# Kernel optimization log

Hardware: AMD Instinct MI355X
Metric: run time of the kernel (lower is better)

Reference implementation:

```python
import jax, jax.numpy as jnp
import numpy as np
import math

N_HEADS = 16
ROPE_THETA = 10000.0
NEG_INF = -1e30


def setup_inputs() -> dict:
    key = jax.random.key(0)
    k1, k2, k3, k4 = jax.random.split(key, 4)
    B, S, D = 2, 2048, 2048
    x = jax.random.normal(k1, (B, S, D), dtype=jnp.float32)
    qkv = 0.01 * jax.random.normal(k2, (2 * D, D), dtype=jnp.float32)
    H = N_HEADS
    dh = D // H
    nope = dh // 2
    rope = dh // 2
    wk = 0.01 * jax.random.normal(k3, (H * nope + rope, D), dtype=jnp.float32)
    wo = 0.01 * jax.random.normal(k4, (D, D), dtype=jnp.float32)
    return {"x": x, "qkv": qkv, "wk": wk, "wo": wo}


def _rope_cos_sin(S, dh, rope_dim, dtype):
    # freqs over full dh as in the torch module, then sliced to rope_dim//2 and tiled x2
    freqs = 1.0 / (ROPE_THETA ** (jnp.arange(0, dh, 2).astype(jnp.float32) / dh))
    emb = jnp.arange(S, dtype=jnp.float32)[:, None] * freqs[None, :]  # [S, dh//2]
    cos = jnp.tile(jnp.cos(emb)[:, : rope_dim // 2], (1, 2))[None, None]  # [1,1,S,rope]
    sin = jnp.tile(jnp.sin(emb)[:, : rope_dim // 2], (1, 2))[None, None]
    return cos.astype(dtype), sin.astype(dtype)


def _apply_rope(xq, cos, sin):
    x1, x2 = jnp.split(xq, 2, axis=-1)
    return xq * cos + jnp.concatenate([-x2, x1], axis=-1) * sin


def reference(x, qkv, wk, wo):
    B, S, D = x.shape
    H = N_HEADS
    dh = D // H
    nope = dh // 2
    rope = dh // 2

    QV = x @ qkv.T                              # [B,S,2D]
    Q, V = jnp.split(QV, 2, axis=-1)
    Q = Q.reshape(B, S, H, dh).transpose(0, 2, 1, 3)        # [B,H,S,dh]
    v_heads = V.reshape(B, S, H, dh).transpose(0, 2, 1, 3)  # [B,H,S,dh]
    Qn, Qr = Q[..., :nope], Q[..., nope:]

    K = x @ wk.T                                # [B,S,H*nope+rope]
    Kn = K[..., : H * nope].reshape(B, S, H, nope).transpose(0, 2, 1, 3)  # [B,H,S,nope]
    Kr = K[..., H * nope :].reshape(B, S, 1, rope).transpose(0, 2, 1, 3)  # [B,1,S,rope]

    cos, sin = _rope_cos_sin(S, dh, rope, x.dtype)
    Qr = _apply_rope(Qr, cos, sin)
    Kr = _apply_rope(Kr, cos, sin)

    q_heads = jnp.concatenate([Qn, Qr], axis=-1)                               # [B,H,S,dh]
    k_heads = jnp.concatenate([Kn, jnp.broadcast_to(Kr, (B, H, S, rope))], -1)  # [B,H,S,dh]

    scale = 1.0 / math.sqrt(dh)
    scores = jnp.einsum('bhqd,bhkd->bhqk', q_heads, k_heads) * scale
    mask = jnp.tril(jnp.ones((S, S), dtype=bool))
    scores = jnp.where(mask[None, None], scores, NEG_INF)
    attn = jax.nn.softmax(scores, axis=-1)
    out = jnp.einsum('bhqk,bhkd->bhqd', attn, v_heads)
    out = out.transpose(0, 2, 1, 3).reshape(B, S, D) @ wo.T
    return (out, k_heads, v_heads)
```

## Files before the change

### kernel.cpp

```cpp
#include <hip/hip_runtime.h>
#include <hip/hip_bf16.h>


typedef unsigned short u16;
typedef unsigned int u32;
typedef __bf16 bf16x8 __attribute__((ext_vector_type(8)));
typedef float f32x4 __attribute__((ext_vector_type(4)));

__device__ __forceinline__ u16 f2bf(float x) {
  union { __hip_bfloat16 h; u16 u; } c;
  c.h = __float2bfloat16(x);
  return c.u;
}
__device__ __forceinline__ float bf2f(u16 u) {
  union { u32 u; float f; } c;
  c.u = ((u32)u) << 16;
  return c.f;
}
__device__ __forceinline__ u32 pack2(float a, float b) {
  return (u32)f2bf(a) | ((u32)f2bf(b) << 16);
}
__device__ __forceinline__ f32x4 mfma16(bf16x8 a, bf16x8 b, f32x4 c) {
  return __builtin_amdgcn_mfma_f32_16x16x32_bf16(a, b, c, 0, 0, 0);
}
__device__ __forceinline__ void gload_lds16(const void* g, void* l) {
  __builtin_amdgcn_global_load_lds((__attribute__((address_space(1))) void*)g,
                                   (__attribute__((address_space(3))) void*)l,
                                   16, 0, 0);
}

__global__ __launch_bounds__(256) void cast_all(const float4* __restrict__ x,
                                                const float4* __restrict__ qkv,
                                                const float* __restrict__ wk,
                                                const float4* __restrict__ wo,
                                                u16* __restrict__ x_bf,
                                                u16* __restrict__ wcomb,
                                                u16* __restrict__ wo_bf) {
  int i = blockIdx.x * blockDim.x + threadIdx.x;
  const float4* src;
  u16* dst;
  int j;
  if (i < 2097152) {
    src = x; dst = x_bf; j = i;
  } else if (i < 4194304) {
    src = qkv; dst = wcomb; j = i - 2097152;
  } else if (i < 4849664) {
    j = i - 4194304;
    int r = (j * 4) >> 11;
    u32 lo = 0, hi = 0;
    if (r < 1088) {
      float4 v = ((const float4*)wk)[j];
      lo = pack2(v.x, v.y);
      hi = pack2(v.z, v.w);
    }
    ((uint2*)(wcomb + 8388608))[j] = make_uint2(lo, hi);
    return;
  } else {
    src = wo; dst = wo_bf; j = i - 4849664;
  }
  float4 v = src[j];
  ((uint2*)dst)[j] = make_uint2(pack2(v.x, v.y), pack2(v.z, v.w));
}

__device__ __forceinline__ void cstore(u16* C, size_t i, float v) { C[i] = f2bf(v); }
__device__ __forceinline__ void cstore(float* C, size_t i, float v) { C[i] = v; }

template <typename CT, int BM, int BN>
__global__ __launch_bounds__(512, 2) void gemm256(const u16* __restrict__ A,
                                                  const u16* __restrict__ W,
                                                  CT* __restrict__ C,
                                                  int M, int N, int K) {
  constexpr int MI = BM / 64;
  constexpr int NI = BN / 128;
  constexpr int AH = BM * 64;
  constexpr int BH = BN * 64;
  constexpr int AL = BM / 128;
  constexpr int BL = BN / 128;
  constexpr int BOFF = 4 * AH;
  __shared__ char lds[BOFF + 4 * BH];
  const int tid = threadIdx.x;
  const int wid = tid >> 6, lane = tid & 63;
  const int lr = lane & 15, lg = lane >> 4;
  const int wr = wid >> 2, wc = wid & 3;
  const int xorv = (lr & 7) << 4;
  const int nwg = gridDim.x * gridDim.y;
  const int lin = blockIdx.y * gridDim.x + blockIdx.x;
  const int swz = (lin & 7) * (nwg >> 3) + (lin >> 3);
  const int m0 = (swz / gridDim.x) * BM;
  const int n0 = (swz % gridDim.x) * BN;
  const int nkt = K >> 6;

  f32x4 acc[2 * MI][2 * NI] = {};
  bf16x8 a[MI][2], b[2 * NI][2];

  const int o0 = tid * 16, o1 = 8192 + tid * 16;
  const int r0 = o0 >> 7, c0 = ((o0 & 127) ^ ((r0 & 7) << 4)) >> 1;
  const int r1 = o1 >> 7, c1 = ((o1 & 127) ^ ((r1 & 7) << 4)) >> 1;
  const u16* gA0[2] = {A + (size_t)(m0 + r0) * K + c0,
                       A + (size_t)(m0 + BM / 2 + r0) * K + c0};
  const u16* gA1[2] = {A + (size_t)(m0 + r1) * K + c1,
                       A + (size_t)(m0 + BM / 2 + r1) * K + c1};
  const u16* gB0[2] = {W + (size_t)(n0 + r0) * K + c0,
                       W + (size_t)(n0 + BN / 2 + r0) * K + c0};
  const u16* gB1[2] = {W + (size_t)(n0 + r1) * K + c1,
                       W + (size_t)(n0 + BN / 2 + r1) * K + c1};

  auto STAGEA = [&](int t, int h) {
    char* d_ = lds + (t & 1) * (2 * AH) + h * AH + wid * 1024;
    gload_lds16(gA0[h] + (size_t)t * 64, d_);
    if constexpr (AL == 2) gload_lds16(gA1[h] + (size_t)t * 64, d_ + 8192);
  };
  auto STAGEB = [&](int t, int h) {
    char* d_ = lds + BOFF + (t & 1) * (2 * BH) + h * BH + wid * 1024;
    gload_lds16(gB0[h] + (size_t)t * 64, d_);
    if constexpr (BL == 2) gload_lds16(gB1[h] + (size_t)t * 64, d_ + 8192);
  };
  auto WAITKEEP = [&]() {
    if constexpr (AL + BL == 4) asm volatile("s_waitcnt vmcnt(4)" ::: "memory");
    else asm volatile("s_waitcnt vmcnt(3)" ::: "memory");
  };

  STAGEA(0, 0); STAGEB(0, 0); STAGEA(0, 1); STAGEB(0, 1);
  if (nkt > 1) { STAGEA(1, 0); STAGEB(1, 0); }
  WAITKEEP();
  __builtin_amdgcn_s_barrier();

  for (int t = 0; t < nkt; ++t) {
    const char* Ab = lds + (t & 1) * (2 * AH);
    const char* Bb = lds + BOFF + (t & 1) * (2 * BH);
    const int arow = wr * (BM / 4), brow = wc * (BN / 8);
#pragma unroll
    for (int mi = 0; mi < MI; mi++)
#pragma unroll
      for (int ks = 0; ks < 2; ks++)
        a[mi][ks] = *(const bf16x8*)(Ab + (arow + mi * 16 + lr) * 128 + ((lg * 16 + ks * 64) ^ xorv));
#pragma unroll
    for (int ni = 0; ni < NI; ni++)
#pragma unroll
      for (int ks = 0; ks < 2; ks++)
        b[ni][ks] = *(const bf16x8*)(Bb + (brow + ni * 16 + lr) * 128 + ((lg * 16 + ks * 64) ^ xorv));
    if (t + 1 < nkt) STAGEA(t + 1, 1);
    __builtin_amdgcn_s_barrier();
    asm volatile("s_waitcnt lgkmcnt(0)" ::: "memory");
    __builtin_amdgcn_sched_barrier(0);
    __builtin_amdgcn_s_setprio(1);
#pragma unroll
    for (int mi = 0; mi < MI; mi++)
#pragma unroll
      for (int ni = 0; ni < NI; ni++)
#pragma unroll
        for (int ks = 0; ks < 2; ks++)
          acc[mi][ni] = mfma16(a[mi][ks], b[ni][ks], acc[mi][ni]);
    __builtin_amdgcn_s_setprio(0);
    __builtin_amdgcn_s_barrier();
#pragma unroll
    for (int ni = 0; ni < NI; ni++)
#pragma unroll
      for (int ks = 0; ks < 2; ks++)
        b[NI + ni][ks] = *(const bf16x8*)(Bb + BH + (brow + ni * 16 + lr) * 128 + ((lg * 16 + ks * 64) ^ xorv));
    if (t + 1 < nkt) STAGEB(t + 1, 1);
    __builtin_amdgcn_s_barrier();
    asm volatile("s_waitcnt lgkmcnt(0)" ::: "memory");
    __builtin_amdgcn_sched_barrier(0);
    __builtin_amdgcn_s_setprio(1);
#pragma unroll
    for (int mi = 0; mi < MI; mi++)
#pragma unroll
      for (int ni = 0; ni < NI; ni++)
#pragma unroll
        for (int ks = 0; ks < 2; ks++)
          acc[mi][NI + ni] = mfma16(a[mi][ks], b[NI + ni][ks], acc[mi][NI + ni]);
    __builtin_amdgcn_s_setprio(0);
    __builtin_amdgcn_s_barrier();
#pragma unroll
    for (int mi = 0; mi < MI; mi++)
#pragma unroll
      for (int ks = 0; ks < 2; ks++)
        a[mi][ks] = *(const bf16x8*)(Ab + AH + (arow + mi * 16 + lr) * 128 + ((lg * 16 + ks * 64) ^ xorv));
    if (t + 2 < nkt) STAGEA(t + 2, 0);
    __builtin_amdgcn_s_barrier();
    asm volatile("s_waitcnt lgkmcnt(0)" ::: "memory");
    __builtin_amdgcn_sched_barrier(0);
    __builtin_amdgcn_s_setprio(1);
#pragma unroll
    for (int mi = 0; mi < MI; mi++)
#pragma unroll
      for (int ni = 0; ni < NI; ni++)
#pragma unroll
        for (int ks = 0; ks < 2; ks++)
          acc[MI + mi][ni] = mfma16(a[mi][ks], b[ni][ks], acc[MI + mi][ni]);
    __builtin_amdgcn_s_setprio(0);
    __builtin_amdgcn_s_barrier();
    if (t + 2 < nkt) {
      STAGEB(t + 2, 0);
      WAITKEEP();
    } else if (t + 1 < nkt) {
      asm volatile("s_waitcnt vmcnt(0)" ::: "memory");
    }
    __builtin_amdgcn_s_barrier();
    asm volatile("s_waitcnt lgkmcnt(0)" ::: "memory");
    __builtin_amdgcn_sched_barrier(0);
    __builtin_amdgcn_s_setprio(1);
#pragma unroll
    for (int mi = 0; mi < MI; mi++)
#pragma unroll
      for (int ni = 0; ni < NI; ni++)
#pragma unroll
        for (int ks = 0; ks < 2; ks++)
          acc[MI + mi][NI + ni] = mfma16(a[mi][ks], b[NI + ni][ks], acc[MI + mi][NI + ni]);
    __builtin_amdgcn_s_setprio(0);
    __builtin_amdgcn_s_barrier();
  }

#pragma unroll
  for (int Mh = 0; Mh < 2; Mh++)
#pragma unroll
    for (int mi = 0; mi < MI; mi++) {
      int row = m0 + Mh * (BM / 2) + wr * (BM / 4) + mi * 16 + lg * 4;
#pragma unroll
      for (int Nh = 0; Nh < 2; Nh++)
#pragma unroll
        for (int ni = 0; ni < NI; ni++) {
          int col = n0 + Nh * (BN / 2) + wc * (BN / 8) + ni * 16 + lr;
#pragma unroll
          for (int r = 0; r < 4; r++)
            cstore(C, (size_t)(row + r) * N + col, acc[Mh * MI + mi][Nh * NI + ni][r]);
        }
    }
}

__global__ __launch_bounds__(256) void rope_scatter2(u16* __restrict__ QVK,
                                                     u16* __restrict__ kh,
                                                     float* __restrict__ k_out, int S) {
  const int row = blockIdx.x;
  const int b = row >> 11, s = row & 2047;
  const int tid = threadIdx.x;
  __shared__ float kr[64];
  const float LOG1E4_64 = 0.14391156511f;
  u16* qrow = QVK + (size_t)row * 5376;
  if (tid < 32) {
    float freq = __expf(-(float)tid * LOG1E4_64);
    float sn, c;
    __sincosf((float)s * freq, &sn, &c);
    float a = bf2f(qrow[5120 + tid]);
    float bb = bf2f(qrow[5152 + tid]);
    kr[tid] = a * c - bb * sn;
    kr[tid + 32] = bb * c + a * sn;
  }
  for (int idx = tid; idx < 512; idx += 256) {
    int h = idx >> 5, jj = idx & 31;
    float freq = __expf(-(float)jj * LOG1E4_64);
    float sn, c;
    __sincosf((float)s * freq, &sn, &c);
    u16* p1 = qrow + h * 128 + 64 + jj;
    u16* p2 = qrow + h * 128 + 96 + jj;
    float x1 = bf2f(*p1), x2 = bf2f(*p2);
    *p1 = f2bf(x1 * c - x2 * sn);
    *p2 = f2bf(x2 * c + x1 * sn);
  }
  __syncthreads();
  for (int idx = tid; idx < 2048; idx += 256) {
    int h = idx >> 7, d = idx & 127;
    float val = (d < 64) ? bf2f(qrow[4096 + h * 64 + d]) : kr[d - 64];
    size_t o = ((size_t)(b * 16 + h) * S + s) * 128 + d;
    kh[o] = f2bf(val);
    k_out[o] = val;
  }
}

__global__ __launch_bounds__(256) void v_scatter(const u16* __restrict__ QVK,
                                                 u16* __restrict__ vt,
                                                 float* __restrict__ v_out, int S) {
  const int blk = blockIdx.x;
  const int st = blk & 63;
  const int dt = (blk >> 6) & 3;
  const int bh = blk >> 8;
  const int b = bh >> 4, h = bh & 15;
  __shared__ u16 t[32][34];
  const int tx = threadIdx.x & 31, ty = threadIdx.x >> 5;
  const int s0 = st * 32, d0 = dt * 32;
#pragma unroll
  for (int i = 0; i < 4; i++) {
    int sl = ty + 8 * i;
    u16 u = QVK[(size_t)(b * S + s0 + sl) * 5376 + 2048 + h * 128 + d0 + tx];
    t[sl][tx] = u;
    v_out[((size_t)bh * S + s0 + sl) * 128 + d0 + tx] = bf2f(u);
  }
  __syncthreads();
#pragma unroll
  for (int i = 0; i < 4; i++) {
    int dl = ty + 8 * i;
    vt[((size_t)bh * 128 + d0 + dl) * S + s0 + tx] = t[tx][dl];
  }
}

__global__ __launch_bounds__(512) void flash_attn4(const u16* __restrict__ QVK,
                                                   const u16* __restrict__ Kh,
                                                   const u16* __restrict__ Vt,
                                                   u16* __restrict__ attn, int S) {
  __shared__ char lds[49152 + 8 * 2304];
  const int tid = threadIdx.x, wid = tid >> 6, lane = tid & 63;
  const int bh = blockIdx.x & 31;
  const int qb = 15 - (int)(blockIdx.x >> 5);
  const int q0 = qb * 128 + wid * 16;
  const int b = bh >> 4, h = bh & 15;
  const int q = lane & 15, g = lane >> 4;
  const u16* Qb = QVK + (size_t)b * S * 5376 + h * 128;
  const u16* Kb = Kh + (size_t)bh * S * 128;
  const u16* Vb = Vt + (size_t)bh * 128 * S;
  const int qg = q0 + q;
  const int xr = (q & 7) << 4;
  char* const Pw = lds + 49152 + wid * 2304 + q * 144;

  const u16* srcK[2];
  const u16* srcV[2];
#pragma unroll
  for (int i = 0; i < 2; i++) {
    int o = ((i * 8 + wid) << 10) | (lane << 4);
    int rK = o >> 8, cbK = (o & 255) ^ ((rK & 7) << 4);
    srcK[i] = Kb + rK * 128 + (cbK >> 1);
    int dV = o >> 7, kbV = (o & 127) ^ ((dV & 7) << 4);
    srcV[i] = Vb + (size_t)dV * S + (kbV >> 1);
  }

  bf16x8 qf[4];
#pragma unroll
  for (int f = 0; f < 4; f++)
    qf[f] = *(const bf16x8*)(Qb + (size_t)qg * 5376 + f * 32 + g * 8);

  f32x4 acc[8] = {};
  float m = -INFINITY, l = 0.f;
  const float sc = 0.08838834764831845f;
  const int ktiles = 2 * qb + 2;

#pragma unroll
  for (int i = 0; i < 2; i++) {
    char* ld = lds + ((i * 8 + wid) << 10);
    gload_lds16(srcK[i], ld);
    gload_lds16(srcV[i], ld + 32768);
  }
  asm volatile("s_waitcnt vmcnt(0)" ::: "memory");
  __builtin_amdgcn_s_barrier();

  for (int kt = 0; kt < ktiles; ++kt) {
    const char* Kt = lds + (kt & 1) * 16384;
    const char* Vl = lds + 32768;
    const bool more = (kt + 1 < ktiles);
    if (more) {
#pragma unroll
      for (int i = 0; i < 2; i++)
        gload_lds16(srcK[i] + (size_t)(kt + 1) * 8192,
                    lds + (((kt & 1) ^ 1) << 14) + ((i * 8 + wid) << 10));
      asm volatile("s_waitcnt vmcnt(4)" ::: "memory");
    } else {
      asm volatile("s_waitcnt vmcnt(2)" ::: "memory");
    }
    __builtin_amdgcn_s_barrier();

    f32x4 s[4] = {};
    const char* Kq = Kt + q * 256;
    __builtin_amdgcn_s_setprio(1);
#pragma unroll
    for (int f = 0; f < 4; f++) {
#pragma unroll
      for (int c = 0; c < 4; c++) {
        bf16x8 kf = *(const bf16x8*)(Kq + c * 4096 + ((f * 64 + g * 16) ^ xr));
        s[c] = mfma16(kf, qf[f], s[c]);
      }
    }
    __builtin_amdgcn_s_setprio(0);

    const int kbg = kt * 64;
    float v[16];
    const bool maskt = (kbg + 63 > q0);
#pragma unroll
    for (int c = 0; c < 4; c++)
#pragma unroll
      for (int r = 0; r < 4; r++) {
        float x = s[c][r];
        if (maskt && (kbg + c * 16 + g * 4 + r > qg)) x = -1e30f;
        v[c * 4 + r] = x;
      }
    float tm = v[0];
#pragma unroll
    for (int i = 1; i < 16; i++) tm = fmaxf(tm, v[i]);
    tm = fmaxf(tm, __shfl_xor(tm, 16));
    tm = fmaxf(tm, __shfl_xor(tm, 32));
    if (!__all(tm <= m + 64.0f)) {
      float mnew = fmaxf(m, tm);
      float corr = __expf((m - mnew) * sc);
      m = mnew;
      l *= corr;
      float corr_r[4];
#pragma unroll
      for (int r = 0; r < 4; r++)
        corr_r[r] = __shfl(corr, (lane & 48) | (g * 4 + r));
#pragma unroll
      for (int j = 0; j < 8; j++)
#pragma unroll
        for (int r = 0; r < 4; r++) acc[j][r] *= corr_r[r];
    }
    const float nms = -m * sc;
    float p[16], ts = 0.f;
#pragma unroll
    for (int i = 0; i < 16; i++) {
      p[i] = __expf(fmaf(v[i], sc, nms));
      ts += p[i];
    }
    ts += __shfl_xor(ts, 16);
    ts += __shfl_xor(ts, 32);
    l += ts;

#pragma unroll
    for (int c = 0; c < 4; c++) {
      int off = (c * 32 + g * 8) ^ xr;
      *(uint2*)(Pw + off) = make_uint2(pack2(p[c * 4], p[c * 4 + 1]),
                                       pack2(p[c * 4 + 2], p[c * 4 + 3]));
    }
    asm volatile("s_waitcnt lgkmcnt(0)" ::: "memory");
    __builtin_amdgcn_sched_barrier(0);
    bf16x8 pcA = *(const bf16x8*)(Pw + ((g * 16) ^ xr));
    bf16x8 pcB = *(const bf16x8*)(Pw + ((64 + g * 16) ^ xr));

    if (more) asm volatile("s_waitcnt vmcnt(2)" ::: "memory");
    else      asm volatile("s_waitcnt vmcnt(0)" ::: "memory");
    __builtin_amdgcn_s_barrier();

    const int vcolA = (g * 16) ^ xr;
    const int vcolB = (64 + g * 16) ^ xr;
    __builtin_amdgcn_s_setprio(1);
#pragma unroll
    for (int j = 0; j < 8; j++) {
      bf16x8 vfA = *(const bf16x8*)(Vl + (j * 16 + q) * 128 + vcolA);
      acc[j] = mfma16(pcA, vfA, acc[j]);
    }
#pragma unroll
    for (int j = 0; j < 8; j++) {
      bf16x8 vfB = *(const bf16x8*)(Vl + (j * 16 + q) * 128 + vcolB);
      acc[j] = mfma16(pcB, vfB, acc[j]);
    }
    __builtin_amdgcn_s_setprio(0);

    __builtin_amdgcn_s_barrier();
    if (more) {
#pragma unroll
      for (int i = 0; i < 2; i++)
        gload_lds16(srcV[i] + (size_t)(kt + 1) * 64,
                    lds + 32768 + ((i * 8 + wid) << 10));
    }
  }

  float linv = 1.0f / l;
  float linv_r[4];
#pragma unroll
  for (int r = 0; r < 4; r++)
    linv_r[r] = __shfl(linv, (lane & 48) | (g * 4 + r));
  u16* ab = attn + (size_t)(b * S + q0) * 2048 + h * 128;
#pragma unroll
  for (int j = 0; j < 8; j++)
#pragma unroll
    for (int r = 0; r < 4; r++)
      ab[(size_t)(g * 4 + r) * 2048 + j * 16 + q] = f2bf(acc[j][r] * linv_r[r]);
}

extern "C" void kernel_launch(void* const* d_in, const int* in_sizes, int n_in,
                              void* d_out, int out_size, void* d_ws, size_t ws_size,
                              hipStream_t stream) {
  (void)in_sizes; (void)n_in; (void)out_size; (void)ws_size;
  const int S = 2048;
  const float* x = (const float*)d_in[0];
  const float* qkv = (const float*)d_in[1];
  const float* wk = (const float*)d_in[2];
  const float* wo = (const float*)d_in[3];
  float* out = (float*)d_out;
  float* k_out = out + (size_t)8388608;
  float* v_out = out + (size_t)16777216;

  char* ws = (char*)d_ws;
  u16* x_bf  = (u16*)(ws + 0);
  u16* wcomb = (u16*)(ws + 16777216);
  u16* wo_bf = (u16*)(ws + 38797312);
  u16* qvk   = (u16*)(ws + 47185920);
  u16* vt_bf = (u16*)(ws + 91226112);
  u16* attn_bf = x_bf;
  u16* k_bf = wcomb;

  cast_all<<<23040, 256, 0, stream>>>((const float4*)x, (const float4*)qkv, wk,
                                      (const float4*)wo, x_bf, wcomb, wo_bf);

  gemm256<u16, 256, 256><<<dim3(16, 16), 512, 0, stream>>>(x_bf, wcomb, qvk,
                                                           4096, 5376, 2048);
  gemm256<u16, 256, 128><<<dim3(10, 16), 512, 0, stream>>>(
      x_bf, wcomb + (size_t)4096 * 2048, qvk + 4096, 4096, 5376, 2048);
  rope_scatter2<<<4096, 256, 0, stream>>>(qvk, k_bf, k_out, S);
  v_scatter<<<8192, 256, 0, stream>>>(qvk, vt_bf, v_out, S);
  flash_attn4<<<512, 512, 0, stream>>>(qvk, k_bf, vt_bf, attn_bf, S);
  gemm256<float, 128, 256><<<dim3(8, 32), 512, 0, stream>>>(attn_bf, wo_bf, out,
                                                            4096, 2048, 2048);
}
```

Baseline: 279.6 us.

## Rewrite flash attention with 32x32 MFMA tiles and 4 waves per block

The attention kernel moves from 16x16x32 to 32x32x16 bf16 MFMA. Each of 4 waves now handles 32 query rows instead of 8 waves handling 16 rows. P now stays in registers as the A operand rather than taking an LDS round trip, and waves skip fully masked causal tiles. The aim is fewer LDS reads per FLOP and less per-wave overhead. The cost is fewer waves per block, which may hurt latency hiding, and more register pressure from the larger accumulators.

Result: no change. 275.6 us (-1.4%).

```diff
diff --git a/kernel.cpp b/kernel.cpp
--- a/kernel.cpp
+++ b/kernel.cpp
@@ -6,6 +6,7 @@
 typedef unsigned int u32;
 typedef __bf16 bf16x8 __attribute__((ext_vector_type(8)));
 typedef float f32x4 __attribute__((ext_vector_type(4)));
+typedef float f32x16 __attribute__((ext_vector_type(16)));
 
 __device__ __forceinline__ u16 f2bf(float x) {
   union { __hip_bfloat16 h; u16 u; } c;
@@ -22,6 +23,9 @@
 }
 __device__ __forceinline__ f32x4 mfma16(bf16x8 a, bf16x8 b, f32x4 c) {
   return __builtin_amdgcn_mfma_f32_16x16x32_bf16(a, b, c, 0, 0, 0);
+}
+__device__ __forceinline__ f32x16 mfma32(bf16x8 a, bf16x8 b, f32x16 c) {
+  return __builtin_amdgcn_mfma_f32_32x32x16_bf16(a, b, c, 0, 0, 0);
 }
 __device__ __forceinline__ void gload_lds16(const void* g, void* l) {
   __builtin_amdgcn_global_load_lds((__attribute__((address_space(1))) void*)g,
@@ -294,48 +298,47 @@
   }
 }
 
-__global__ __launch_bounds__(512) void flash_attn4(const u16* __restrict__ QVK,
+__global__ __launch_bounds__(256) void flash_attn6(const u16* __restrict__ QVK,
                                                    const u16* __restrict__ Kh,
                                                    const u16* __restrict__ Vt,
                                                    u16* __restrict__ attn, int S) {
-  __shared__ char lds[49152 + 8 * 2304];
+  __shared__ char lds[49664];
   const int tid = threadIdx.x, wid = tid >> 6, lane = tid & 63;
   const int bh = blockIdx.x & 31;
   const int qb = 15 - (int)(blockIdx.x >> 5);
-  const int q0 = qb * 128 + wid * 16;
+  const int q0w = qb * 128 + wid * 32;
   const int b = bh >> 4, h = bh & 15;
-  const int q = lane & 15, g = lane >> 4;
+  const int r32 = lane & 31, hh = lane >> 5;
   const u16* Qb = QVK + (size_t)b * S * 5376 + h * 128;
   const u16* Kb = Kh + (size_t)bh * S * 128;
   const u16* Vb = Vt + (size_t)bh * 128 * S;
-  const int qg = q0 + q;
-  const int xr = (q & 7) << 4;
-  char* const Pw = lds + 49152 + wid * 2304 + q * 144;
-
-  const u16* srcK[2];
-  const u16* srcV[2];
-#pragma unroll
-  for (int i = 0; i < 2; i++) {
-    int o = ((i * 8 + wid) << 10) | (lane << 4);
+  const int qg = q0w + r32;
+  const int xr = (r32 & 7) << 4;
+  char* const Pc = lds + 49152 + wid * 128;
+
+  const u16 *srcK[4], *srcV[4];
+#pragma unroll
+  for (int i = 0; i < 4; i++) {
+    int o = i * 4096 + tid * 16;
     int rK = o >> 8, cbK = (o & 255) ^ ((rK & 7) << 4);
     srcK[i] = Kb + rK * 128 + (cbK >> 1);
     int dV = o >> 7, kbV = (o & 127) ^ ((dV & 7) << 4);
     srcV[i] = Vb + (size_t)dV * S + (kbV >> 1);
   }
 
-  bf16x8 qf[4];
-#pragma unroll
-  for (int f = 0; f < 4; f++)
-    qf[f] = *(const bf16x8*)(Qb + (size_t)qg * 5376 + f * 32 + g * 8);
-
-  f32x4 acc[8] = {};
+  bf16x8 qf[8];
+#pragma unroll
+  for (int f = 0; f < 8; f++)
+    qf[f] = *(const bf16x8*)(Qb + (size_t)qg * 5376 + f * 16 + hh * 8);
+
+  f32x16 acc[4] = {};
   float m = -INFINITY, l = 0.f;
   const float sc = 0.08838834764831845f;
   const int ktiles = 2 * qb + 2;
 
 #pragma unroll
-  for (int i = 0; i < 2; i++) {
-    char* ld = lds + ((i * 8 + wid) << 10);
+  for (int i = 0; i < 4; i++) {
+    char* ld = lds + i * 4096 + wid * 1024;
     gload_lds16(srcK[i], ld);
     gload_lds16(srcV[i], ld + 32768);
   }
@@ -348,119 +351,139 @@
     const bool more = (kt + 1 < ktiles);
     if (more) {
 #pragma unroll
-      for (int i = 0; i < 2; i++)
+      for (int i = 0; i < 4; i++)
         gload_lds16(srcK[i] + (size_t)(kt + 1) * 8192,
-                    lds + (((kt & 1) ^ 1) << 14) + ((i * 8 + wid) << 10));
+                    lds + (((kt & 1) ^ 1) << 14) + i * 4096 + wid * 1024);
+      asm volatile("s_waitcnt vmcnt(8)" ::: "memory");
+    } else {
       asm volatile("s_waitcnt vmcnt(4)" ::: "memory");
-    } else {
-      asm volatile("s_waitcnt vmcnt(2)" ::: "memory");
-    }
-    __builtin_amdgcn_s_barrier();
-
-    f32x4 s[4] = {};
-    const char* Kq = Kt + q * 256;
-    __builtin_amdgcn_s_setprio(1);
-#pragma unroll
-    for (int f = 0; f < 4; f++) {
-#pragma unroll
-      for (int c = 0; c < 4; c++) {
-        bf16x8 kf = *(const bf16x8*)(Kq + c * 4096 + ((f * 64 + g * 16) ^ xr));
-        s[c] = mfma16(kf, qf[f], s[c]);
+    }
+    __builtin_amdgcn_s_barrier();
+
+    const int kbg = kt * 64;
+    const bool active = (kbg <= q0w + 31);
+    u32 u[16];
+    if (active) {
+      f32x16 s[2] = {};
+      __builtin_amdgcn_s_setprio(1);
+#pragma unroll
+      for (int kg = 0; kg < 2; kg++) {
+        const char* Kq = Kt + (kg * 32 + r32) * 256;
+#pragma unroll
+        for (int f = 0; f < 8; f++) {
+          bf16x8 kf = *(const bf16x8*)(Kq + ((f * 32 + hh * 16) ^ xr));
+          s[kg] = mfma32(kf, qf[f], s[kg]);
+        }
       }
-    }
-    __builtin_amdgcn_s_setprio(0);
-
-    const int kbg = kt * 64;
-    float v[16];
-    const bool maskt = (kbg + 63 > q0);
-#pragma unroll
-    for (int c = 0; c < 4; c++)
-#pragma unroll
-      for (int r = 0; r < 4; r++) {
-        float x = s[c][r];
-        if (maskt && (kbg + c * 16 + g * 4 + r > qg)) x = -1e30f;
-        v[c * 4 + r] = x;
+      __builtin_amdgcn_s_setprio(0);
+      const bool maskt = (kbg + 63 > q0w);
+      if (maskt) {
+#pragma unroll
+        for (int kg = 0; kg < 2; kg++)
+#pragma unroll
+          for (int r = 0; r < 16; r++)
+            if (kbg + kg * 32 + (r & 3) + 8 * (r >> 2) + 4 * hh > qg)
+              s[kg][r] = -1e30f;
       }
-    float tm = v[0];
-#pragma unroll
-    for (int i = 1; i < 16; i++) tm = fmaxf(tm, v[i]);
-    tm = fmaxf(tm, __shfl_xor(tm, 16));
-    tm = fmaxf(tm, __shfl_xor(tm, 32));
-    if (!__all(tm <= m + 64.0f)) {
-      float mnew = fmaxf(m, tm);
-      float corr = __expf((m - mnew) * sc);
-      m = mnew;
-      l *= corr;
-      float corr_r[4];
-#pragma unroll
-      for (int r = 0; r < 4; r++)
-        corr_r[r] = __shfl(corr, (lane & 48) | (g * 4 + r));
-#pragma unroll
-      for (int j = 0; j < 8; j++)
-#pragma unroll
-        for (int r = 0; r < 4; r++) acc[j][r] *= corr_r[r];
-    }
-    const float nms = -m * sc;
-    float p[16], ts = 0.f;
-#pragma unroll
-    for (int i = 0; i < 16; i++) {
-      p[i] = __expf(fmaf(v[i], sc, nms));
-      ts += p[i];
-    }
-    ts += __shfl_xor(ts, 16);
-    ts += __shfl_xor(ts, 32);
-    l += ts;
-
-#pragma unroll
-    for (int c = 0; c < 4; c++) {
-      int off = (c * 32 + g * 8) ^ xr;
-      *(uint2*)(Pw + off) = make_uint2(pack2(p[c * 4], p[c * 4 + 1]),
-                                       pack2(p[c * 4 + 2], p[c * 4 + 3]));
-    }
-    asm volatile("s_waitcnt lgkmcnt(0)" ::: "memory");
-    __builtin_amdgcn_sched_barrier(0);
-    bf16x8 pcA = *(const bf16x8*)(Pw + ((g * 16) ^ xr));
-    bf16x8 pcB = *(const bf16x8*)(Pw + ((64 + g * 16) ^ xr));
-
-    if (more) asm volatile("s_waitcnt vmcnt(2)" ::: "memory");
+      float tm = s[0][0];
+#pragma unroll
+      for (int r = 1; r < 16; r++) tm = fmaxf(tm, s[0][r]);
+#pragma unroll
+      for (int r = 0; r < 16; r++) tm = fmaxf(tm, s[1][r]);
+      tm = fmaxf(tm, __shfl_xor(tm, 32));
+      if (!__all(tm <= m + 64.0f)) {
+        float mnew = fmaxf(m, tm);
+        float corr = __expf((m - mnew) * sc);
+        m = mnew;
+        l *= corr;
+        if (lane < 32) *(float*)(Pc + r32 * 4) = corr;
+        asm volatile("s_waitcnt lgkmcnt(0)" ::: "memory");
+        __builtin_amdgcn_sched_barrier(0);
+        f32x4 c0 = *(const f32x4*)(Pc + (4 * hh) * 4);
+        f32x4 c1 = *(const f32x4*)(Pc + (8 + 4 * hh) * 4);
+        f32x4 c2 = *(const f32x4*)(Pc + (16 + 4 * hh) * 4);
+        f32x4 c3 = *(const f32x4*)(Pc + (24 + 4 * hh) * 4);
+#pragma unroll
+        for (int dg = 0; dg < 4; dg++)
+#pragma unroll
+          for (int r = 0; r < 16; r++) {
+            float cr = (r >> 2) == 0 ? c0[r & 3]
+                     : (r >> 2) == 1 ? c1[r & 3]
+                     : (r >> 2) == 2 ? c2[r & 3] : c3[r & 3];
+            acc[dg][r] *= cr;
+          }
+      }
+      const float nms = -m * sc;
+      float ts = 0.f;
+#pragma unroll
+      for (int kg = 0; kg < 2; kg++)
+#pragma unroll
+        for (int r = 0; r < 16; r++) {
+          float pv = __expf(fmaf(s[kg][r], sc, nms));
+          s[kg][r] = pv;
+          ts += pv;
+        }
+      ts += __shfl_xor(ts, 32);
+      l += ts;
+#pragma unroll
+      for (int kg = 0; kg < 2; kg++)
+#pragma unroll
+        for (int i = 0; i < 8; i++)
+          u[kg * 8 + i] = pack2(s[kg][2 * i], s[kg][2 * i + 1]);
+    }
+
+    if (more) asm volatile("s_waitcnt vmcnt(4)" ::: "memory");
     else      asm volatile("s_waitcnt vmcnt(0)" ::: "memory");
     __builtin_amdgcn_s_barrier();
 
-    const int vcolA = (g * 16) ^ xr;
-    const int vcolB = (64 + g * 16) ^ xr;
-    __builtin_amdgcn_s_setprio(1);
-#pragma unroll
-    for (int j = 0; j < 8; j++) {
-      bf16x8 vfA = *(const bf16x8*)(Vl + (j * 16 + q) * 128 + vcolA);
-      acc[j] = mfma16(pcA, vfA, acc[j]);
-    }
-#pragma unroll
-    for (int j = 0; j < 8; j++) {
-      bf16x8 vfB = *(const bf16x8*)(Vl + (j * 16 + q) * 128 + vcolB);
-      acc[j] = mfma16(pcB, vfB, acc[j]);
-    }
-    __builtin_amdgcn_s_setprio(0);
-
+    if (active) {
+      __builtin_amdgcn_s_setprio(1);
+#pragma unroll
+      for (int dg = 0; dg < 4; dg++) {
+        const char* Vq = Vl + (dg * 32 + r32) * 128;
+#pragma unroll
+        for (int ss = 0; ss < 4; ss++) {
+          uint2 vlo = *(const uint2*)(Vq + ((ss * 32 + 8 * hh) ^ xr));
+          uint2 vhi = *(const uint2*)(Vq + ((ss * 32 + 16 + 8 * hh) ^ xr));
+          union { u32 w[4]; bf16x8 v; } vb, pa;
+          vb.w[0] = vlo.x; vb.w[1] = vlo.y; vb.w[2] = vhi.x; vb.w[3] = vhi.y;
+          pa.w[0] = u[ss * 4 + 0];
+          pa.w[1] = u[ss * 4 + 1];
+          pa.w[2] = u[ss * 4 + 2];
+          pa.w[3] = u[ss * 4 + 3];
+          acc[dg] = mfma32(pa.v, vb.v, acc[dg]);
+        }
+      }
+      __builtin_amdgcn_s_setprio(0);
+    }
     __builtin_amdgcn_s_barrier();
     if (more) {
 #pragma unroll
-      for (int i = 0; i < 2; i++)
+      for (int i = 0; i < 4; i++)
         gload_lds16(srcV[i] + (size_t)(kt + 1) * 64,
-                    lds + 32768 + ((i * 8 + wid) << 10));
+                    lds + 32768 + i * 4096 + wid * 1024);
     }
   }
 
   float linv = 1.0f / l;
-  float linv_r[4];
-#pragma unroll
-  for (int r = 0; r < 4; r++)
-    linv_r[r] = __shfl(linv, (lane & 48) | (g * 4 + r));
-  u16* ab = attn + (size_t)(b * S + q0) * 2048 + h * 128;
-#pragma unroll
-  for (int j = 0; j < 8; j++)
-#pragma unroll
-    for (int r = 0; r < 4; r++)
-      ab[(size_t)(g * 4 + r) * 2048 + j * 16 + q] = f2bf(acc[j][r] * linv_r[r]);
+  if (lane < 32) *(float*)(Pc + r32 * 4) = linv;
+  asm volatile("s_waitcnt lgkmcnt(0)" ::: "memory");
+  __builtin_amdgcn_sched_barrier(0);
+  f32x4 l0 = *(const f32x4*)(Pc + (4 * hh) * 4);
+  f32x4 l1 = *(const f32x4*)(Pc + (8 + 4 * hh) * 4);
+  f32x4 l2 = *(const f32x4*)(Pc + (16 + 4 * hh) * 4);
+  f32x4 l3 = *(const f32x4*)(Pc + (24 + 4 * hh) * 4);
+  u16* ab = attn + (size_t)(b * S + q0w) * 2048 + h * 128;
+#pragma unroll
+  for (int dg = 0; dg < 4; dg++)
+#pragma unroll
+    for (int r = 0; r < 16; r++) {
+      int rowl = (r & 3) + 8 * (r >> 2) + 4 * hh;
+      float li = (r >> 2) == 0 ? l0[r & 3]
+               : (r >> 2) == 1 ? l1[r & 3]
+               : (r >> 2) == 2 ? l2[r & 3] : l3[r & 3];
+      ab[(size_t)rowl * 2048 + dg * 32 + r32] = f2bf(acc[dg][r] * li);
+    }
 }
 
 extern "C" void kernel_launch(void* const* d_in, const int* in_sizes, int n_in,
@@ -494,7 +517,7 @@
       x_bf, wcomb + (size_t)4096 * 2048, qvk + 4096, 4096, 5376, 2048);
   rope_scatter2<<<4096, 256, 0, stream>>>(qvk, k_bf, k_out, S);
   v_scatter<<<8192, 256, 0, stream>>>(qvk, vt_bf, v_out, S);
-  flash_attn4<<<512, 512, 0, stream>>>(qvk, k_bf, vt_bf, attn_bf, S);
+  flash_attn6<<<512, 256, 0, stream>>>(qvk, k_bf, vt_bf, attn_bf, S);
   gemm256<float, 128, 256><<<dim3(8, 32), 512, 0, stream>>>(attn_bf, wo_bf, out,
                                                             4096, 2048, 2048);
 }
```
